# Kernel tuning notes

Hardware: AMD Instinct MI355X
Metric: run time of the kernel (lower is better)

## Reference

```python
import jax, jax.numpy as jnp
from jax import lax
import numpy as np

VOCAB, EMB, H, T, B = 2500, 64, 64, 512, 256


def _gru_dir(x, mask, Wi, Wh, b, reverse):
    """Keras GRU (reset_after=True) over [B,T,D] with boolean mask [B,T].
    Masked steps carry state unchanged (Keras masking semantics; GRU output==state)."""
    bi, bh = b[0], b[1]
    if reverse:
        x = jnp.flip(x, 1)
        mask = jnp.flip(mask, 1)
    xp = x @ Wi + bi  # [B,T,3H], precompute input projections once

    def step(h, inp):
        xp_t, m_t = inp
        rec = h @ Wh + bh
        xz, xr, xh = jnp.split(xp_t, 3, axis=-1)
        rz, rr, rh = jnp.split(rec, 3, axis=-1)
        z = jax.nn.sigmoid(xz + rz)
        r = jax.nn.sigmoid(xr + rr)
        hh = jnp.tanh(xh + r * rh)
        h_new = z * h + (1.0 - z) * hh
        h = jnp.where(m_t, h_new, h)
        return h, h

    h0 = jnp.zeros((x.shape[0], Wh.shape[0]), x.dtype)
    hT, ys = lax.scan(step, h0, (jnp.swapaxes(xp, 0, 1), jnp.swapaxes(mask, 0, 1)[..., None]))
    ys = jnp.swapaxes(ys, 0, 1)  # [B,T,H]
    if reverse:
        ys = jnp.flip(ys, 1)
    return ys, hT


def _bigru_seq(x, mask, Wif, Whf, bf, Wib, Whb, bb):
    yf, _ = _gru_dir(x, mask, Wif, Whf, bf, False)
    yb, _ = _gru_dir(x, mask, Wib, Whb, bb, True)
    return jnp.concatenate([yf, yb], axis=-1)  # [B,T,2H]


def setup_inputs() -> dict:
    key = jax.random.key(0)
    ks = iter(jax.random.split(key, 40))
    s = 0.05
    d = {"tokens": jax.random.randint(next(ks), (B, T), 0, VOCAB)}
    d["emb"] = jax.random.normal(next(ks), (VOCAB, EMB), jnp.float32) * s
    for l, din in ((1, EMB), (2, 2 * H), (3, 2 * H)):
        for dr in ("f", "b"):
            d[f"wi{l}{dr}"] = jax.random.normal(next(ks), (din, 3 * H), jnp.float32) * s
            d[f"wh{l}{dr}"] = jax.random.normal(next(ks), (H, 3 * H), jnp.float32) * s
            d[f"bb{l}{dr}"] = jax.random.normal(next(ks), (2, 3 * H), jnp.float32) * s
    d["wd1"] = jax.random.normal(next(ks), (2 * H, 64), jnp.float32) * s
    d["bd1"] = jnp.zeros((64,), jnp.float32)
    d["wd2"] = jax.random.normal(next(ks), (64, 64), jnp.float32) * s
    d["bd2"] = jnp.zeros((64,), jnp.float32)
    d["wd3"] = jax.random.normal(next(ks), (64, 64), jnp.float32) * s
    d["bd3"] = jnp.zeros((64,), jnp.float32)
    d["wo"] = jax.random.normal(next(ks), (64, 28), jnp.float32) * s
    d["bo"] = jnp.zeros((28,), jnp.float32)
    return d


def reference(tokens, emb, wi1f, wh1f, bb1f, wi1b, wh1b, bb1b,
              wi2f, wh2f, bb2f, wi2b, wh2b, bb2b,
              wi3f, wh3f, bb3f, wi3b, wh3b, bb3b,
              wd1, bd1, wd2, bd2, wd3, bd3, wo, bo):
    mask = tokens > 0  # mask_zero=True
    x = emb[tokens]  # [B,T,EMB]
    x = _bigru_seq(x, mask, wi1f, wh1f, bb1f, wi1b, wh1b, bb1b)
    x = _bigru_seq(x, mask, wi2f, wh2f, bb2f, wi2b, wh2b, bb2b)
    _, hf = _gru_dir(x, mask, wi3f, wh3f, bb3f, False)
    _, hb = _gru_dir(x, mask, wi3b, wh3b, bb3b, True)
    x = jnp.concatenate([hf, hb], axis=-1)  # [B,2H]
    x = jax.nn.relu(x @ wd1 + bd1)
    x = jax.nn.relu(x @ wd2 + bd2)
    x = jax.nn.relu(x @ wd3 + bd3)
    return jax.nn.sigmoid(x @ wo + bo)  # [B,28]
```

## Files before the change

kernel.cpp:

```cpp
#include <hip/hip_runtime.h>
#include <hip/hip_bf16.h>
#include <cstddef>

#define T_SEQ 512
#define BATCH 256
#define RTOT (BATCH * T_SEQ)

__device__ __forceinline__ float fsigmoid(float x) {
    return 1.0f / (1.0f + __expf(-x));
}
__device__ __forceinline__ float ftanh(float x) {
    return 1.0f - 2.0f / (__expf(2.0f * x) + 1.0f);
}

template <int DIN, bool EMBED>
__global__ __launch_bounds__(192) void proj_kernel(
    const float* __restrict__ X, const int* __restrict__ tokens,
    const float* __restrict__ emb,
    const float* __restrict__ Wf, const float* __restrict__ bf_,
    const float* __restrict__ Wb, const float* __restrict__ bb_,
    float* __restrict__ xpf, float* __restrict__ xpb)
{
    constexpr int ROWS = 32;
    constexpr int PAD = 36;
    __shared__ __align__(16) float xt[DIN][PAD];
    const int r0 = blockIdx.x * ROWS;
    const int tid = threadIdx.x;

    for (int e = tid; e < ROWS * DIN; e += 192) {
        const int row = e / DIN;
        const int i = e % DIN;
        float v;
        if (EMBED) {
            v = emb[(size_t)tokens[r0 + row] * 64 + i];
        } else {
            v = X[(size_t)(r0 + row) * DIN + i];
        }
        xt[i][row] = v;
    }
    __syncthreads();

    const int col = tid;
    #pragma unroll
    for (int d = 0; d < 2; d++) {
        const float* __restrict__ W = d ? Wb : Wf;
        const float* __restrict__ bi = d ? bb_ : bf_;
        float* __restrict__ outp = d ? xpb : xpf;
        float acc[ROWS];
        const float b0 = bi[col];
        #pragma unroll
        for (int r = 0; r < ROWS; r++) acc[r] = b0;
        #pragma unroll 4
        for (int i = 0; i < DIN; i++) {
            const float w = W[i * 192 + col];
            #pragma unroll
            for (int r = 0; r < ROWS; r += 4) {
                const float4 x4 = *(const float4*)&xt[i][r];
                acc[r + 0] = fmaf(x4.x, w, acc[r + 0]);
                acc[r + 1] = fmaf(x4.y, w, acc[r + 1]);
                acc[r + 2] = fmaf(x4.z, w, acc[r + 2]);
                acc[r + 3] = fmaf(x4.w, w, acc[r + 3]);
            }
        }
        #pragma unroll
        for (int r = 0; r < ROWS; r++) {
            outp[(size_t)(r0 + r) * 192 + col] = acc[r];
        }
    }
}

__global__ __launch_bounds__(192) void gru_scan(
    const float* __restrict__ xpf, const float* __restrict__ xpb,
    const float* __restrict__ whf, const float* __restrict__ whb,
    const float* __restrict__ bbf, const float* __restrict__ bbb,
    const int* __restrict__ tokens,
    float* __restrict__ y,
    float* __restrict__ hfinal)
{
    const int chain = blockIdx.x;
    const int b = chain >> 1;
    const int dir = chain & 1;
    const float* __restrict__ xp = dir ? xpb : xpf;
    const float* __restrict__ wh = dir ? whb : whf;
    const float* __restrict__ bb = dir ? bbb : bbf;
    const int k = threadIdx.x;

    float whk[64];
    #pragma unroll
    for (int i = 0; i < 64; i++) whk[i] = wh[i * 192 + k];
    const float bhk = bb[192 + k];

    __shared__ __align__(16) float h_lds[64];
    __shared__ float z_lds[64];
    __shared__ float r_lds[64];
    if (k < 64) h_lds[k] = 0.0f;
    __syncthreads();

    const int t0 = dir ? (T_SEQ - 1) : 0;
    const int st = dir ? -1 : 1;
    const size_t base = (size_t)b * T_SEQ;

    float xv = xp[(base + t0) * 192 + k];
    int tok = tokens[base + t0];

    for (int t = 0; t < T_SEQ; t++) {
        const int tn = (t + 1 < T_SEQ) ? (t + 1) : t;
        const int te_n = t0 + st * tn;
        const float xv_n = xp[(base + te_n) * 192 + k];
        const int tok_n = tokens[base + te_n];

        float acc = bhk;
        #pragma unroll
        for (int i = 0; i < 64; i += 4) {
            const float4 h4 = *(const float4*)&h_lds[i];
            acc = fmaf(h4.x, whk[i + 0], acc);
            acc = fmaf(h4.y, whk[i + 1], acc);
            acc = fmaf(h4.z, whk[i + 2], acc);
            acc = fmaf(h4.w, whk[i + 3], acc);
        }
        if (k < 64) {
            z_lds[k] = fsigmoid(xv + acc);
        } else if (k < 128) {
            r_lds[k - 64] = fsigmoid(xv + acc);
        }
        __syncthreads();
        if (k >= 128) {
            const int j = k - 128;
            const float r = r_lds[j];
            const float hh = ftanh(xv + r * acc);
            const float z = z_lds[j];
            const float hold = h_lds[j];
            float hnew = z * hold + (1.0f - z) * hh;
            if (!(tok > 0)) hnew = hold;
            h_lds[j] = hnew;
            if (y) {
                const int te = t0 + st * t;
                y[(base + te) * 128 + (dir << 6) + j] = hnew;
            }
        }
        __syncthreads();
        xv = xv_n;
        tok = tok_n;
    }
    if (hfinal && k >= 128) {
        hfinal[b * 128 + (dir << 6) + (k - 128)] = h_lds[k - 128];
    }
}

__global__ __launch_bounds__(64) void mlp_kernel(
    const float* __restrict__ hcat,
    const float* __restrict__ wd1, const float* __restrict__ bd1,
    const float* __restrict__ wd2, const float* __restrict__ bd2,
    const float* __restrict__ wd3, const float* __restrict__ bd3,
    const float* __restrict__ wo, const float* __restrict__ bo,
    float* __restrict__ outp)
{
    const int b = blockIdx.x;
    const int j = threadIdx.x;
    __shared__ float x0[128];
    __shared__ float x1[64];
    x0[j] = hcat[b * 128 + j];
    x0[j + 64] = hcat[b * 128 + 64 + j];
    __syncthreads();
    float a = bd1[j];
    #pragma unroll 4
    for (int i = 0; i < 128; i++) a = fmaf(x0[i], wd1[i * 64 + j], a);
    a = fmaxf(a, 0.0f);
    x1[j] = a;
    __syncthreads();
    float a2 = bd2[j];
    #pragma unroll 4
    for (int i = 0; i < 64; i++) a2 = fmaf(x1[i], wd2[i * 64 + j], a2);
    a2 = fmaxf(a2, 0.0f);
    __syncthreads();
    x1[j] = a2;
    __syncthreads();
    float a3 = bd3[j];
    #pragma unroll 4
    for (int i = 0; i < 64; i++) a3 = fmaf(x1[i], wd3[i * 64 + j], a3);
    a3 = fmaxf(a3, 0.0f);
    __syncthreads();
    x1[j] = a3;
    __syncthreads();
    if (j < 28) {
        float o = bo[j];
        #pragma unroll 4
        for (int i = 0; i < 64; i++) o = fmaf(x1[i], wo[i * 28 + j], o);
        outp[b * 28 + j] = fsigmoid(o);
    }
}

extern "C" void kernel_launch(void* const* d_in, const int* in_sizes, int n_in,
                              void* d_out, int out_size, void* d_ws, size_t ws_size,
                              hipStream_t stream)
{
    const int* tokens  = (const int*)d_in[0];
    const float* emb   = (const float*)d_in[1];
    const float* wi1f  = (const float*)d_in[2];
    const float* wh1f  = (const float*)d_in[3];
    const float* bb1f  = (const float*)d_in[4];
    const float* wi1b  = (const float*)d_in[5];
    const float* wh1b  = (const float*)d_in[6];
    const float* bb1b  = (const float*)d_in[7];
    const float* wi2f  = (const float*)d_in[8];
    const float* wh2f  = (const float*)d_in[9];
    const float* bb2f  = (const float*)d_in[10];
    const float* wi2b  = (const float*)d_in[11];
    const float* wh2b  = (const float*)d_in[12];
    const float* bb2b  = (const float*)d_in[13];
    const float* wi3f  = (const float*)d_in[14];
    const float* wh3f  = (const float*)d_in[15];
    const float* bb3f  = (const float*)d_in[16];
    const float* wi3b  = (const float*)d_in[17];
    const float* wh3b  = (const float*)d_in[18];
    const float* bb3b  = (const float*)d_in[19];
    const float* wd1   = (const float*)d_in[20];
    const float* bd1   = (const float*)d_in[21];
    const float* wd2   = (const float*)d_in[22];
    const float* bd2   = (const float*)d_in[23];
    const float* wd3   = (const float*)d_in[24];
    const float* bd3   = (const float*)d_in[25];
    const float* wo    = (const float*)d_in[26];
    const float* bo    = (const float*)d_in[27];

    float* y    = (float*)d_ws;
    float* xpf  = y + (size_t)RTOT * 128;
    float* xpb  = xpf + (size_t)RTOT * 192;
    float* hcat = y;

    const dim3 pb(192), pg(RTOT / 32);

    proj_kernel<64, true><<<pg, pb, 0, stream>>>(nullptr, tokens, emb,
                                                 wi1f, bb1f, wi1b, bb1b, xpf, xpb);
    gru_scan<<<512, 192, 0, stream>>>(xpf, xpb, wh1f, wh1b, bb1f, bb1b,
                                      tokens, y, nullptr);
    proj_kernel<128, false><<<pg, pb, 0, stream>>>(y, nullptr, nullptr,
                                                   wi2f, bb2f, wi2b, bb2b, xpf, xpb);
    gru_scan<<<512, 192, 0, stream>>>(xpf, xpb, wh2f, wh2b, bb2f, bb2b,
                                      tokens, y, nullptr);
    proj_kernel<128, false><<<pg, pb, 0, stream>>>(y, nullptr, nullptr,
                                                   wi3f, bb3f, wi3b, bb3b, xpf, xpb);
    gru_scan<<<512, 192, 0, stream>>>(xpf, xpb, wh3f, wh3b, bb3f, bb3b,
                                      tokens, nullptr, hcat);
    mlp_kernel<<<256, 64, 0, stream>>>(hcat, wd1, bd1, wd2, bd2, wd3, bd3,
                                       wo, bo, (float*)d_out);
}
```

Baseline: 1.542 ms.

## Run each GRU chain in one wavefront computing all three gates per thread

```diff
diff --git a/kernel.cpp b/kernel.cpp
--- a/kernel.cpp
+++ b/kernel.cpp
@@ -69,7 +69,7 @@
     }
 }
 
-__global__ __launch_bounds__(192) void gru_scan(
+__global__ __launch_bounds__(64, 1) void gru_scan_w64(
     const float* __restrict__ xpf, const float* __restrict__ xpb,
     const float* __restrict__ whf, const float* __restrict__ whb,
     const float* __restrict__ bbf, const float* __restrict__ bbb,
@@ -82,69 +82,79 @@
     const int dir = chain & 1;
     const float* __restrict__ xp = dir ? xpb : xpf;
     const float* __restrict__ wh = dir ? whb : whf;
-    const float* __restrict__ bb = dir ? bbb : bbf;
-    const int k = threadIdx.x;
-
-    float whk[64];
+    const float* __restrict__ bbv = dir ? bbb : bbf;
+    const int j = threadIdx.x;
+
+    float wz[64], wr[64], wc[64];
     #pragma unroll
-    for (int i = 0; i < 64; i++) whk[i] = wh[i * 192 + k];
-    const float bhk = bb[192 + k];
+    for (int i = 0; i < 64; i++) {
+        wz[i] = wh[i * 192 + j];
+        wr[i] = wh[i * 192 + 64 + j];
+        wc[i] = wh[i * 192 + 128 + j];
+    }
+    const float bhz = bbv[192 + j];
+    const float bhr = bbv[192 + 64 + j];
+    const float bhc = bbv[192 + 128 + j];
 
     __shared__ __align__(16) float h_lds[64];
-    __shared__ float z_lds[64];
-    __shared__ float r_lds[64];
-    if (k < 64) h_lds[k] = 0.0f;
+    __shared__ float m_lds[T_SEQ];
+    const size_t base = (size_t)b * T_SEQ;
+    #pragma unroll
+    for (int u = 0; u < T_SEQ / 64; u++) {
+        const int tk = tokens[base + u * 64 + j];
+        m_lds[u * 64 + j] = (tk > 0) ? 1.0f : 0.0f;
+    }
+    h_lds[j] = 0.0f;
+    float h = 0.0f;
     __syncthreads();
 
     const int t0 = dir ? (T_SEQ - 1) : 0;
     const int st = dir ? -1 : 1;
-    const size_t base = (size_t)b * T_SEQ;
-
-    float xv = xp[(base + t0) * 192 + k];
-    int tok = tokens[base + t0];
-
+    const float* xrow = xp + (base + t0) * 192;
+    float xz0 = xrow[j], xr0 = xrow[64 + j], xc0 = xrow[128 + j];
+    const float* xrow1 = xrow + st * 192;
+    float xz1 = xrow1[j], xr1 = xrow1[64 + j], xc1 = xrow1[128 + j];
+
+    float* yp = y ? (y + (base + t0) * 128 + (dir << 6) + j) : nullptr;
+    const ptrdiff_t ystep = (ptrdiff_t)st * 128;
+    int mt = t0;
+
+    #pragma unroll 2
     for (int t = 0; t < T_SEQ; t++) {
-        const int tn = (t + 1 < T_SEQ) ? (t + 1) : t;
-        const int te_n = t0 + st * tn;
-        const float xv_n = xp[(base + te_n) * 192 + k];
-        const int tok_n = tokens[base + te_n];
-
-        float acc = bhk;
+        const float* rp = (t + 2 < T_SEQ) ? (xrow + 2 * st * 192) : xrow;
+        const float pz = rp[j], pr = rp[64 + j], pc = rp[128 + j];
+        const float m = m_lds[mt];
+
+        float az = bhz, ar = bhr, ac = bhc;
         #pragma unroll
         for (int i = 0; i < 64; i += 4) {
             const float4 h4 = *(const float4*)&h_lds[i];
-            acc = fmaf(h4.x, whk[i + 0], acc);
-            acc = fmaf(h4.y, whk[i + 1], acc);
-            acc = fmaf(h4.z, whk[i + 2], acc);
-            acc = fmaf(h4.w, whk[i + 3], acc);
-        }
-        if (k < 64) {
-            z_lds[k] = fsigmoid(xv + acc);
-        } else if (k < 128) {
-            r_lds[k - 64] = fsigmoid(xv + acc);
-        }
-        __syncthreads();
-        if (k >= 128) {
-            const int j = k - 128;
-            const float r = r_lds[j];
-            const float hh = ftanh(xv + r * acc);
-            const float z = z_lds[j];
-            const float hold = h_lds[j];
-            float hnew = z * hold + (1.0f - z) * hh;
-            if (!(tok > 0)) hnew = hold;
-            h_lds[j] = hnew;
-            if (y) {
-                const int te = t0 + st * t;
-                y[(base + te) * 128 + (dir << 6) + j] = hnew;
-            }
-        }
-        __syncthreads();
-        xv = xv_n;
-        tok = tok_n;
-    }
-    if (hfinal && k >= 128) {
-        hfinal[b * 128 + (dir << 6) + (k - 128)] = h_lds[k - 128];
-    }
+            az = fmaf(h4.x, wz[i + 0], az);
+            ar = fmaf(h4.x, wr[i + 0], ar);
+            ac = fmaf(h4.x, wc[i + 0], ac);
+            az = fmaf(h4.y, wz[i + 1], az);
+            ar = fmaf(h4.y, wr[i + 1], ar);
+            ac = fmaf(h4.y, wc[i + 1], ac);
+            az = fmaf(h4.z, wz[i + 2], az);
+            ar = fmaf(h4.z, wr[i + 2], ar);
+            ac = fmaf(h4.z, wc[i + 2], ac);
+            az = fmaf(h4.w, wz[i + 3], az);
+            ar = fmaf(h4.w, wr[i + 3], ar);
+            ac = fmaf(h4.w, wc[i + 3], ac);
+        }
+        const float z  = fsigmoid(xz0 + az);
+        const float r  = fsigmoid(xr0 + ar);
+        const float hh = ftanh(xc0 + r * ac);
+        const float hnew = z * h + (1.0f - z) * hh;
+        h = fmaf(m, hnew - h, h);
+        if (yp) { *yp = h; yp += ystep; }
+        h_lds[j] = h;
+        xz0 = xz1; xr0 = xr1; xc0 = xc1;
+        xz1 = pz;  xr1 = pr;  xc1 = pc;
+        xrow += st * 192;
+        mt += st;
+    }
+    if (hfinal) hfinal[b * 128 + (dir << 6) + j] = h;
 }
 
 __global__ __launch_bounds__(64) void mlp_kernel(
@@ -232,16 +242,16 @@
 
     proj_kernel<64, true><<<pg, pb, 0, stream>>>(nullptr, tokens, emb,
                                                  wi1f, bb1f, wi1b, bb1b, xpf, xpb);
-    gru_scan<<<512, 192, 0, stream>>>(xpf, xpb, wh1f, wh1b, bb1f, bb1b,
-                                      tokens, y, nullptr);
+    gru_scan_w64<<<512, 64, 0, stream>>>(xpf, xpb, wh1f, wh1b, bb1f, bb1b,
+                                         tokens, y, nullptr);
     proj_kernel<128, false><<<pg, pb, 0, stream>>>(y, nullptr, nullptr,
                                                    wi2f, bb2f, wi2b, bb2b, xpf, xpb);
-    gru_scan<<<512, 192, 0, stream>>>(xpf, xpb, wh2f, wh2b, bb2f, bb2b,
-                                      tokens, y, nullptr);
+    gru_scan_w64<<<512, 64, 0, stream>>>(xpf, xpb, wh2f, wh2b, bb2f, bb2b,
+                                         tokens, y, nullptr);
     proj_kernel<128, false><<<pg, pb, 0, stream>>>(y, nullptr, nullptr,
                                                    wi3f, bb3f, wi3b, bb3b, xpf, xpb);
-    gru_scan<<<512, 192, 0, stream>>>(xpf, xpb, wh3f, wh3b, bb3f, bb3b,
-                                      tokens, nullptr, hcat);
+    gru_scan_w64<<<512, 64, 0, stream>>>(xpf, xpb, wh3f, wh3b, bb3f, bb3b,
+                                         tokens, nullptr, hcat);
     mlp_kernel<<<256, 64, 0, stream>>>(hcat, wd1, bd1, wd2, bd2, wd3, bd3,
                                        wo, bo, (float*)d_out);
 }
```

After: 1.633 ms. 5.9% more time.

## Batch 16 GRU chains per block and compute recurrence with bf16 MFMA

Applied to the files above, without the earlier changes.

```diff
diff --git a/kernel.cpp b/kernel.cpp
--- a/kernel.cpp
+++ b/kernel.cpp
@@ -6,11 +6,19 @@
 #define BATCH 256
 #define RTOT (BATCH * T_SEQ)
 
+typedef __attribute__((ext_vector_type(8))) short bf16x8;
+typedef __attribute__((ext_vector_type(4))) float f32x4;
+
 __device__ __forceinline__ float fsigmoid(float x) {
     return 1.0f / (1.0f + __expf(-x));
 }
 __device__ __forceinline__ float ftanh(float x) {
     return 1.0f - 2.0f / (__expf(2.0f * x) + 1.0f);
+}
+__device__ __forceinline__ unsigned short f2bf(float f) {
+    union { float f; unsigned u; } v; v.f = f;
+    const unsigned r = (v.u + 0x7fffu + ((v.u >> 16) & 1u)) >> 16;
+    return (unsigned short)r;
 }
 
 template <int DIN, bool EMBED>
@@ -69,7 +77,7 @@
     }
 }
 
-__global__ __launch_bounds__(192) void gru_scan(
+__global__ __launch_bounds__(256) void gru_scan_mfma(
     const float* __restrict__ xpf, const float* __restrict__ xpb,
     const float* __restrict__ whf, const float* __restrict__ whb,
     const float* __restrict__ bbf, const float* __restrict__ bbb,
@@ -77,73 +85,125 @@
     float* __restrict__ y,
     float* __restrict__ hfinal)
 {
-    const int chain = blockIdx.x;
-    const int b = chain >> 1;
-    const int dir = chain & 1;
+    const int dir = blockIdx.x & 1;
+    const int b0 = (blockIdx.x >> 1) * 16;
     const float* __restrict__ xp = dir ? xpb : xpf;
     const float* __restrict__ wh = dir ? whb : whf;
-    const float* __restrict__ bb = dir ? bbb : bbf;
-    const int k = threadIdx.x;
-
-    float whk[64];
+    const float* __restrict__ bbv = dir ? bbb : bbf;
+
+    const int tid = threadIdx.x;
+    const int w = tid >> 6;
+    const int lane = tid & 63;
+    const int n = lane & 15;
+    const int quad = lane >> 4;
+
+    bf16x8 Bz[2], Br[2], Bc[2];
     #pragma unroll
-    for (int i = 0; i < 64; i++) whk[i] = wh[i * 192 + k];
-    const float bhk = bb[192 + k];
-
-    __shared__ __align__(16) float h_lds[64];
-    __shared__ float z_lds[64];
-    __shared__ float r_lds[64];
-    if (k < 64) h_lds[k] = 0.0f;
-    __syncthreads();
+    for (int h = 0; h < 2; h++) {
+        #pragma unroll
+        for (int j = 0; j < 8; j++) {
+            const int k = quad * 8 + j + 32 * h;
+            const int cb = 16 * w + n;
+            Bz[h][j] = (short)f2bf(wh[k * 192 + cb]);
+            Br[h][j] = (short)f2bf(wh[k * 192 + 64 + cb]);
+            Bc[h][j] = (short)f2bf(wh[k * 192 + 128 + cb]);
+        }
+    }
+    const float bhz = bbv[192 + 16 * w + n];
+    const float bhr = bbv[192 + 64 + 16 * w + n];
+    const float bhc = bbv[192 + 128 + 16 * w + n];
+
+    __shared__ __align__(16) unsigned short Hb[2][16][64];
+    __shared__ float msk[16][T_SEQ];
+
+    for (int i = tid; i < 16 * T_SEQ; i += 256) {
+        const int c = i >> 9, t = i & (T_SEQ - 1);
+        msk[c][t] = (tokens[(size_t)(b0 + c) * T_SEQ + t] > 0) ? 1.0f : 0.0f;
+    }
+    for (int i = tid; i < 16 * 64; i += 256) {
+        ((unsigned short*)Hb[0])[i] = 0;
+    }
 
     const int t0 = dir ? (T_SEQ - 1) : 0;
     const int st = dir ? -1 : 1;
-    const size_t base = (size_t)b * T_SEQ;
-
-    float xv = xp[(base + t0) * 192 + k];
-    int tok = tokens[base + t0];
-
+
+    float h[4] = {0.f, 0.f, 0.f, 0.f};
+    size_t xrow[4];
+    float* yptr[4];
+    #pragma unroll
+    for (int r = 0; r < 4; r++) {
+        const int chain = quad * 4 + r;
+        xrow[r] = ((size_t)(b0 + chain) * T_SEQ + t0) * 192;
+        yptr[r] = y ? (y + ((size_t)(b0 + chain) * T_SEQ + t0) * 128
+                         + (dir << 6) + 16 * w + n) : nullptr;
+    }
+    const ptrdiff_t ystep = (ptrdiff_t)st * 128;
+    const int cz = 16 * w + n, cr = 64 + 16 * w + n, cc = 128 + 16 * w + n;
+
+    float xz[4], xr[4], xc[4];
+    #pragma unroll
+    for (int r = 0; r < 4; r++) {
+        xz[r] = xp[xrow[r] + cz];
+        xr[r] = xp[xrow[r] + cr];
+        xc[r] = xp[xrow[r] + cc];
+    }
+
+    __syncthreads();
+
+    int p = 0;
+    int te = t0;
     for (int t = 0; t < T_SEQ; t++) {
-        const int tn = (t + 1 < T_SEQ) ? (t + 1) : t;
-        const int te_n = t0 + st * tn;
-        const float xv_n = xp[(base + te_n) * 192 + k];
-        const int tok_n = tokens[base + te_n];
-
-        float acc = bhk;
-        #pragma unroll
-        for (int i = 0; i < 64; i += 4) {
-            const float4 h4 = *(const float4*)&h_lds[i];
-            acc = fmaf(h4.x, whk[i + 0], acc);
-            acc = fmaf(h4.y, whk[i + 1], acc);
-            acc = fmaf(h4.z, whk[i + 2], acc);
-            acc = fmaf(h4.w, whk[i + 3], acc);
-        }
-        if (k < 64) {
-            z_lds[k] = fsigmoid(xv + acc);
-        } else if (k < 128) {
-            r_lds[k - 64] = fsigmoid(xv + acc);
+        const bf16x8 A0 = *(const bf16x8*)&Hb[p][n][quad * 8];
+        const bf16x8 A1 = *(const bf16x8*)&Hb[p][n][32 + quad * 8];
+
+        f32x4 az = {bhz, bhz, bhz, bhz};
+        f32x4 ar = {bhr, bhr, bhr, bhr};
+        f32x4 ac = {bhc, bhc, bhc, bhc};
+        az = __builtin_amdgcn_mfma_f32_16x16x32_bf16(A0, Bz[0], az, 0, 0, 0);
+        ar = __builtin_amdgcn_mfma_f32_16x16x32_bf16(A0, Br[0], ar, 0, 0, 0);
+        ac = __builtin_amdgcn_mfma_f32_16x16x32_bf16(A0, Bc[0], ac, 0, 0, 0);
+        az = __builtin_amdgcn_mfma_f32_16x16x32_bf16(A1, Bz[1], az, 0, 0, 0);
+        ar = __builtin_amdgcn_mfma_f32_16x16x32_bf16(A1, Br[1], ar, 0, 0, 0);
+        ac = __builtin_amdgcn_mfma_f32_16x16x32_bf16(A1, Bc[1], ac, 0, 0, 0);
+
+        float pz[4], pr[4], pc[4];
+        const ptrdiff_t adv = (t + 1 < T_SEQ) ? (ptrdiff_t)st * 192 : 0;
+        #pragma unroll
+        for (int r = 0; r < 4; r++) {
+            const size_t nrow = xrow[r] + adv;
+            pz[r] = xp[nrow + cz];
+            pr[r] = xp[nrow + cr];
+            pc[r] = xp[nrow + cc];
+            xrow[r] = nrow;
+        }
+
+        #pragma unroll
+        for (int r = 0; r < 4; r++) {
+            const int chain = quad * 4 + r;
+            const float m  = msk[chain][te];
+            const float z  = fsigmoid(xz[r] + az[r]);
+            const float rr = fsigmoid(xr[r] + ar[r]);
+            const float hh = ftanh(xc[r] + rr * ac[r]);
+            const float hn = z * h[r] + (1.0f - z) * hh;
+            h[r] = fmaf(m, hn - h[r], h[r]);
+            if (y) { *yptr[r] = h[r]; yptr[r] += ystep; }
+            Hb[p ^ 1][chain][16 * w + n] = f2bf(h[r]);
         }
         __syncthreads();
-        if (k >= 128) {
-            const int j = k - 128;
-            const float r = r_lds[j];
-            const float hh = ftanh(xv + r * acc);
-            const float z = z_lds[j];
-            const float hold = h_lds[j];
-            float hnew = z * hold + (1.0f - z) * hh;
-            if (!(tok > 0)) hnew = hold;
-            h_lds[j] = hnew;
-            if (y) {
-                const int te = t0 + st * t;
-                y[(base + te) * 128 + (dir << 6) + j] = hnew;
-            }
-        }
-        __syncthreads();
-        xv = xv_n;
-        tok = tok_n;
-    }
-    if (hfinal && k >= 128) {
-        hfinal[b * 128 + (dir << 6) + (k - 128)] = h_lds[k - 128];
+        p ^= 1;
+        te += st;
+        #pragma unroll
+        for (int r = 0; r < 4; r++) {
+            xz[r] = pz[r]; xr[r] = pr[r]; xc[r] = pc[r];
+        }
+    }
+
+    if (hfinal) {
+        #pragma unroll
+        for (int r = 0; r < 4; r++) {
+            const int chain = quad * 4 + r;
+            hfinal[(size_t)(b0 + chain) * 128 + (dir << 6) + 16 * w + n] = h[r];
+        }
     }
 }
 
@@ -232,16 +292,16 @@
 
     proj_kernel<64, true><<<pg, pb, 0, stream>>>(nullptr, tokens, emb,
                                                  wi1f, bb1f, wi1b, bb1b, xpf, xpb);
-    gru_scan<<<512, 192, 0, stream>>>(xpf, xpb, wh1f, wh1b, bb1f, bb1b,
-                                      tokens, y, nullptr);
+    gru_scan_mfma<<<32, 256, 0, stream>>>(xpf, xpb, wh1f, wh1b, bb1f, bb1b,
+                                          tokens, y, nullptr);
     proj_kernel<128, false><<<pg, pb, 0, stream>>>(y, nullptr, nullptr,
                                                    wi2f, bb2f, wi2b, bb2b, xpf, xpb);
-    gru_scan<<<512, 192, 0, stream>>>(xpf, xpb, wh2f, wh2b, bb2f, bb2b,
-                                      tokens, y, nullptr);
+    gru_scan_mfma<<<32, 256, 0, stream>>>(xpf, xpb, wh2f, wh2b, bb2f, bb2b,
+                                          tokens, y, nullptr);
     proj_kernel<128, false><<<pg, pb, 0, stream>>>(y, nullptr, nullptr,
                                                    wi3f, bb3f, wi3b, bb3b, xpf, xpb);
-    gru_scan<<<512, 192, 0, stream>>>(xpf, xpb, wh3f, wh3b, bb3f, bb3b,
-                                      tokens, nullptr, hcat);
+    gru_scan_mfma<<<32, 256, 0, stream>>>(xpf, xpb, wh3f, wh3b, bb3f, bb3b,
+                                          tokens, nullptr, hcat);
     mlp_kernel<<<256, 64, 0, stream>>>(hcat, wd1, bd1, wd2, bd2, wd3, bd3,
                                        wo, bo, (float*)d_out);
 }
```

New measurement: 2.214 ms. 43.6% more time.

## Process two batch rows per GRU scan block with LDS-resident recurrent weights

Applied to the files above, without the earlier changes.

```diff
diff --git a/kernel.cpp b/kernel.cpp
--- a/kernel.cpp
+++ b/kernel.cpp
@@ -69,7 +69,7 @@
     }
 }
 
-__global__ __launch_bounds__(192) void gru_scan(
+__global__ __launch_bounds__(192) void gru_scan2(
     const float* __restrict__ xpf, const float* __restrict__ xpb,
     const float* __restrict__ whf, const float* __restrict__ whb,
     const float* __restrict__ bbf, const float* __restrict__ bbb,
@@ -77,73 +77,107 @@
     float* __restrict__ y,
     float* __restrict__ hfinal)
 {
-    const int chain = blockIdx.x;
-    const int b = chain >> 1;
-    const int dir = chain & 1;
+    const int dir = blockIdx.x & 1;
+    const int b0 = (blockIdx.x >> 1) * 2;
     const float* __restrict__ xp = dir ? xpb : xpf;
     const float* __restrict__ wh = dir ? whb : whf;
-    const float* __restrict__ bb = dir ? bbb : bbf;
-    const int k = threadIdx.x;
-
-    float whk[64];
-    #pragma unroll
-    for (int i = 0; i < 64; i++) whk[i] = wh[i * 192 + k];
-    const float bhk = bb[192 + k];
-
-    __shared__ __align__(16) float h_lds[64];
-    __shared__ float z_lds[64];
-    __shared__ float r_lds[64];
-    if (k < 64) h_lds[k] = 0.0f;
-    __syncthreads();
+    const float* __restrict__ bbv = dir ? bbb : bbf;
+    const int tid = threadIdx.x;
+    const int w = tid >> 6;
+    const int j = tid & 63;
+
+    __shared__ __align__(16) float4 wlds4[16 * 192];
+    __shared__ __align__(16) float2 hp[64];
+    __shared__ __align__(16) float2 zp[64];
+    __shared__ __align__(16) float2 rp[64];
+    __shared__ __align__(16) float2 mp[T_SEQ];
+
+    #pragma unroll 4
+    for (int i = 0; i < 16; i++) {
+        float4 w4;
+        w4.x = wh[(4 * i + 0) * 192 + tid];
+        w4.y = wh[(4 * i + 1) * 192 + tid];
+        w4.z = wh[(4 * i + 2) * 192 + tid];
+        w4.w = wh[(4 * i + 3) * 192 + tid];
+        wlds4[i * 192 + tid] = w4;
+    }
+    for (int i = tid; i < T_SEQ * 2; i += 192) {
+        const int t = i >> 1, c = i & 1;
+        ((float*)mp)[i] =
+            (tokens[(size_t)(b0 + c) * T_SEQ + t] > 0) ? 1.0f : 0.0f;
+    }
+    if (w == 0) { hp[j].x = 0.0f; hp[j].y = 0.0f; }
+    const float bh = bbv[192 + tid];
+    float h0 = 0.0f, h1 = 0.0f;
 
     const int t0 = dir ? (T_SEQ - 1) : 0;
     const int st = dir ? -1 : 1;
-    const size_t base = (size_t)b * T_SEQ;
-
-    float xv = xp[(base + t0) * 192 + k];
-    int tok = tokens[base + t0];
+    const ptrdiff_t rstep = (ptrdiff_t)st * 192;
+    const float* xr0 = xp + ((size_t)b0 * T_SEQ + t0) * 192;
+    const float* xr1 = xp + ((size_t)(b0 + 1) * T_SEQ + t0) * 192;
+    float x00 = xr0[tid], x01 = xr1[tid];
+    float x10 = xr0[rstep + tid], x11 = xr1[rstep + tid];
+
+    float* y0 = y ? (y + ((size_t)b0 * T_SEQ + t0) * 128 + (dir << 6) + j)
+                  : nullptr;
+    float* y1 = y ? (y + ((size_t)(b0 + 1) * T_SEQ + t0) * 128 + (dir << 6) + j)
+                  : nullptr;
+    const ptrdiff_t ystep = (ptrdiff_t)st * 128;
+    int te = t0;
+
+    __syncthreads();
 
     for (int t = 0; t < T_SEQ; t++) {
-        const int tn = (t + 1 < T_SEQ) ? (t + 1) : t;
-        const int te_n = t0 + st * tn;
-        const float xv_n = xp[(base + te_n) * 192 + k];
-        const int tok_n = tokens[base + te_n];
-
-        float acc = bhk;
+        const ptrdiff_t adv = (t + 2 < T_SEQ) ? 2 * rstep : 0;
+        const float p0 = xr0[adv + tid];
+        const float p1 = xr1[adv + tid];
+
+        float a0 = bh, a1 = bh;
         #pragma unroll
-        for (int i = 0; i < 64; i += 4) {
-            const float4 h4 = *(const float4*)&h_lds[i];
-            acc = fmaf(h4.x, whk[i + 0], acc);
-            acc = fmaf(h4.y, whk[i + 1], acc);
-            acc = fmaf(h4.z, whk[i + 2], acc);
-            acc = fmaf(h4.w, whk[i + 3], acc);
-        }
-        if (k < 64) {
-            z_lds[k] = fsigmoid(xv + acc);
-        } else if (k < 128) {
-            r_lds[k - 64] = fsigmoid(xv + acc);
+        for (int i = 0; i < 16; i++) {
+            const float4 w4 = wlds4[i * 192 + tid];
+            const float4 q0 = *(const float4*)&hp[4 * i];
+            const float4 q1 = *(const float4*)&hp[4 * i + 2];
+            a0 = fmaf(w4.x, q0.x, a0); a1 = fmaf(w4.x, q0.y, a1);
+            a0 = fmaf(w4.y, q0.z, a0); a1 = fmaf(w4.y, q0.w, a1);
+            a0 = fmaf(w4.z, q1.x, a0); a1 = fmaf(w4.z, q1.y, a1);
+            a0 = fmaf(w4.w, q1.z, a0); a1 = fmaf(w4.w, q1.w, a1);
+        }
+        if (w == 0) {
+            zp[j].x = fsigmoid(x00 + a0);
+            zp[j].y = fsigmoid(x01 + a1);
+        } else if (w == 1) {
+            rp[j].x = fsigmoid(x00 + a0);
+            rp[j].y = fsigmoid(x01 + a1);
         }
         __syncthreads();
-        if (k >= 128) {
-            const int j = k - 128;
-            const float r = r_lds[j];
-            const float hh = ftanh(xv + r * acc);
-            const float z = z_lds[j];
-            const float hold = h_lds[j];
-            float hnew = z * hold + (1.0f - z) * hh;
-            if (!(tok > 0)) hnew = hold;
-            h_lds[j] = hnew;
+        if (w == 2) {
+            const float2 r2 = rp[j];
+            const float2 z2 = zp[j];
+            const float2 m2 = mp[te];
+            const float hh0 = ftanh(x00 + r2.x * a0);
+            const float hh1 = ftanh(x01 + r2.y * a1);
+            const float hn0 = z2.x * h0 + (1.0f - z2.x) * hh0;
+            const float hn1 = z2.y * h1 + (1.0f - z2.y) * hh1;
+            h0 = fmaf(m2.x, hn0 - h0, h0);
+            h1 = fmaf(m2.y, hn1 - h1, h1);
+            hp[j].x = h0;
+            hp[j].y = h1;
             if (y) {
-                const int te = t0 + st * t;
-                y[(base + te) * 128 + (dir << 6) + j] = hnew;
+                *y0 = h0; y0 += ystep;
+                *y1 = h1; y1 += ystep;
             }
         }
         __syncthreads();
-        xv = xv_n;
-        tok = tok_n;
-    }
-    if (hfinal && k >= 128) {
-        hfinal[b * 128 + (dir << 6) + (k - 128)] = h_lds[k - 128];
+        x00 = x10; x01 = x11;
+        x10 = p0;  x11 = p1;
+        xr0 += rstep;
+        xr1 += rstep;
+        te += st;
+    }
+    if (hfinal && w == 2) {
+        hfinal[(size_t)b0 * 128 + (dir << 6) + j] = h0;
+        hfinal[(size_t)(b0 + 1) * 128 + (dir << 6) + j] = h1;
     }
 }
 
@@ -232,16 +266,16 @@
 
     proj_kernel<64, true><<<pg, pb, 0, stream>>>(nullptr, tokens, emb,
                                                  wi1f, bb1f, wi1b, bb1b, xpf, xpb);
-    gru_scan<<<512, 192, 0, stream>>>(xpf, xpb, wh1f, wh1b, bb1f, bb1b,
-                                      tokens, y, nullptr);
+    gru_scan2<<<256, 192, 0, stream>>>(xpf, xpb, wh1f, wh1b, bb1f, bb1b,
+                                       tokens, y, nullptr);
     proj_kernel<128, false><<<pg, pb, 0, stream>>>(y, nullptr, nullptr,
                                                    wi2f, bb2f, wi2b, bb2b, xpf, xpb);
-    gru_scan<<<512, 192, 0, stream>>>(xpf, xpb, wh2f, wh2b, bb2f, bb2b,
-                                      tokens, y, nullptr);
+    gru_scan2<<<256, 192, 0, stream>>>(xpf, xpb, wh2f, wh2b, bb2f, bb2b,
+                                       tokens, y, nullptr);
     proj_kernel<128, false><<<pg, pb, 0, stream>>>(y, nullptr, nullptr,
                                                    wi3f, bb3f, wi3b, bb3b, xpf, xpb);
-    gru_scan<<<512, 192, 0, stream>>>(xpf, xpb, wh3f, wh3b, bb3f, bb3b,
-                                      tokens, nullptr, hcat);
+    gru_scan2<<<256, 192, 0, stream>>>(xpf, xpb, wh3f, wh3b, bb3f, bb3b,
+                                       tokens, nullptr, hcat);
     mlp_kernel<<<256, 64, 0, stream>>>(hcat, wd1, bd1, wd2, bd2, wd3, bd3,
                                        wo, bo, (float*)d_out);
 }
```

After: 2.089 ms. 1.36x slower.
